# Optimization experiments

Hardware: AMD Instinct MI355X
Metric: run time of the kernel (lower is better)

Reference implementation:

```python
import jax, jax.numpy as jnp
import numpy as np

N = 20000   # nodes
E = 320000  # edges (before self-loops)
D = 256     # feature width (inChl = hdChl = outChl)
H = 4       # heads
C = D // H  # per-head channels = 64
NEG_SLOPE = 0.2
LN_EPS = 1e-5


def setup_inputs() -> dict:
    key = jax.random.key(0)
    ks = jax.random.split(key, 2 + 4 * 4)
    inp = {}
    inp["x"] = jax.random.normal(ks[0], (1, N, D), dtype=jnp.float32)
    inp["edge_index"] = jax.random.randint(ks[1], (2, E), 0, N, dtype=jnp.int32)
    s = 1.0 / np.sqrt(D)
    for i in range(4):
        k = 2 + 4 * i
        inp[f"Wl{i+1}"] = (jax.random.normal(ks[k], (D, H * C), dtype=jnp.float32) * s)
        inp[f"Wr{i+1}"] = (jax.random.normal(ks[k + 1], (D, H * C), dtype=jnp.float32) * s)
        inp[f"att{i+1}"] = (jax.random.normal(ks[k + 2], (H, C), dtype=jnp.float32) * s)
        inp[f"b{i+1}"] = jnp.zeros((H * C,), dtype=jnp.float32)
        inp[f"g{i+1}"] = jnp.ones((D,), dtype=jnp.float32)
        inp[f"be{i+1}"] = jnp.zeros((D,), dtype=jnp.float32)
    return inp


def _segment_softmax(scores, seg, num_segments):
    # scores: [E, H], per-destination softmax over incoming edges
    m = jax.ops.segment_max(scores, seg, num_segments=num_segments)
    e = jnp.exp(scores - m[seg])
    d = jax.ops.segment_sum(e, seg, num_segments=num_segments)
    return e / d[seg]


def _gatv2(x, src, dst, Wl, Wr, att, b):
    # GATv2Conv defaults: share_weights=False, concat=True, negative_slope=0.2
    n = x.shape[0]
    xl = (x @ Wl).reshape(n, H, C)  # source transform
    xr = (x @ Wr).reshape(n, H, C)  # target transform
    m = xl[src] + xr[dst]                                  # [E', H, C]
    e = jnp.sum(jax.nn.leaky_relu(m, NEG_SLOPE) * att, -1) # [E', H]
    alpha = _segment_softmax(e, dst, n)                    # [E', H]
    out = jax.ops.segment_sum(xl[src] * alpha[:, :, None], dst, num_segments=n)
    return out.reshape(n, H * C) + b


def _layernorm(x, g, b):
    mu = jnp.mean(x, -1, keepdims=True)
    var = jnp.mean(jnp.square(x - mu), -1, keepdims=True)
    return (x - mu) * jax.lax.rsqrt(var + LN_EPS) * g + b


def _forward(x, edge_index, layers):
    h = x[0]  # squeeze batch dim -> [N, D]
    n = h.shape[0]
    loop = jnp.arange(n, dtype=edge_index.dtype)
    src = jnp.concatenate([edge_index[0], loop])  # add_self_loops=True
    dst = jnp.concatenate([edge_index[1], loop])
    for (Wl, Wr, att, b, g, be) in layers:
        h = _gatv2(h, src, dst, Wl, Wr, att, b)
        h = jax.nn.relu(_layernorm(h, g, be))
    return h[None]  # unsqueeze -> [1, N, D]


def reference(x, edge_index,
              Wl1, Wr1, att1, b1, g1, be1,
              Wl2, Wr2, att2, b2, g2, be2,
              Wl3, Wr3, att3, b3, g3, be3,
              Wl4, Wr4, att4, b4, g4, be4):
    layers = [(Wl1, Wr1, att1, b1, g1, be1),
              (Wl2, Wr2, att2, b2, g2, be2),
              (Wl3, Wr3, att3, b3, g3, be3),
              (Wl4, Wr4, att4, b4, g4, be4)]
    return _forward(x, edge_index, layers)
```

## Files before the change

kernel.cpp:

```cpp
#include <hip/hip_runtime.h>
#include <math.h>

#define N_NODES 20000
#define E_EDGES 320000
#define EP (E_EDGES + N_NODES)
#define D 256
#define NHEAD 4
#define CH 64
#define NEG_SLOPE 0.2f
#define LN_EPS 1e-5f

typedef _Float16 half8_t __attribute__((ext_vector_type(8)));
typedef _Float16 half4_t __attribute__((ext_vector_type(4)));
typedef _Float16 half2_t __attribute__((ext_vector_type(2)));
typedef float   float4_t __attribute__((ext_vector_type(4)));
typedef int     iv4_t    __attribute__((ext_vector_type(4)));

#define SCATTER_BLOCKS ((EP + 255) / 256)
#define CONV_BLOCKS ((N_NODES * D / 4 + 255) / 256)

__device__ __forceinline__ void async_cp16(const void* g, void* l)
{
    __builtin_amdgcn_global_load_lds(
        (const __attribute__((address_space(1))) void*)g,
        (__attribute__((address_space(3))) void*)l, 16, 0, 0);
}

template<int CTRL>
__device__ __forceinline__ float dpp_add(float v) {
    int t = __builtin_amdgcn_update_dpp(0, __float_as_int(v), CTRL, 0xF, 0xF, true);
    return v + __int_as_float(t);
}
__device__ __forceinline__ float grp8_sum(float v) {
    v = dpp_add<0xB1>(v);
    v = dpp_add<0x4E>(v);
    v = dpp_add<0x141>(v);
    return v;
}

__device__ __forceinline__ iv4_t load_idx4(const int* p) {
    iv4_t v;
    __builtin_memcpy(&v, p, 16);
    return v;
}

__device__ __forceinline__ float dot_att8(half8_t t, const half2_t a0, const half2_t a1,
                                          const half2_t a2, const half2_t a3) {
    half2_t t01 = {t[0], t[1]}, t23 = {t[2], t[3]};
    half2_t t45 = {t[4], t[5]}, t67 = {t[6], t[7]};
    float v = __builtin_amdgcn_fdot2(t01, a0, 0.0f, false);
    v = __builtin_amdgcn_fdot2(t23, a1, v, false);
    v = __builtin_amdgcn_fdot2(t45, a2, v, false);
    return __builtin_amdgcn_fdot2(t67, a3, v, false);
}

struct WPtrs { const float* p[8]; };

__global__ __launch_bounds__(256)
void convert_hist_kernel(const float* __restrict__ x, _Float16* __restrict__ h16,
                         const int* __restrict__ ei, int* __restrict__ deg,
                         WPtrs wp, _Float16* __restrict__ Wt_all)
{
    if (blockIdx.x >= CONV_BLOCKS) {
        __shared__ float tile[64][65];
        int bz = blockIdx.x - CONV_BLOCKS;
        int bxi = bz & 3, byi = (bz >> 2) & 3, z = bz >> 4;
        const float* W = wp.p[z];
        _Float16* out = Wt_all + (size_t)z * 65536;
        int bx = bxi * 64, by = byi * 64;
        int t = threadIdx.x;
        #pragma unroll
        for (int i = 0; i < 16; ++i) {
            int idx = t + i * 256;
            int kk = idx >> 6, nn = idx & 63;
            tile[kk][nn] = W[(by + kk) * 256 + bx + nn];
        }
        __syncthreads();
        #pragma unroll
        for (int i = 0; i < 16; ++i) {
            int idx = t + i * 256;
            int nn = idx >> 6, kk = idx & 63;
            out[(bx + nn) * 256 + by + kk] = (_Float16)tile[kk][nn];
        }
        return;
    }
    int i = blockIdx.x * 256 + threadIdx.x;
    if (i < EP) {
        int dst = (i < E_EDGES) ? ei[E_EDGES + i] : (i - E_EDGES);
        atomicAdd(&deg[dst], 1);
    }
    if (i >= N_NODES * D / 4) return;
    float4 v = reinterpret_cast<const float4*>(x)[i];
    half4_t o;
    o.x = (_Float16)v.x; o.y = (_Float16)v.y; o.z = (_Float16)v.z; o.w = (_Float16)v.w;
    reinterpret_cast<half4_t*>(h16)[i] = o;
}

__global__ __launch_bounds__(1024)
void csr_scan_kernel(const int* __restrict__ deg, int* __restrict__ rowptr,
                     int* __restrict__ cursor, int* __restrict__ csr_src)
{
    __shared__ int buf[5120];
    __shared__ int wsum[16];
    __shared__ int carry_s;
    int t = threadIdx.x, lane = t & 63, w = t >> 6;
    if (t == 0) carry_s = 0;
    if (t < 8) csr_src[EP + t] = 0;

    for (int c = 0; c < 4; ++c) {
        int base = c * 5120;
        #pragma unroll
        for (int k = 0; k < 5; ++k) {
            int idx = base + k * 1024 + t;
            buf[k * 1024 + t] = (idx < N_NODES) ? deg[idx] : 0;
        }
        __syncthreads();
        int loc[5]; int s = 0;
        #pragma unroll
        for (int k = 0; k < 5; ++k) { loc[k] = buf[t * 5 + k]; s += loc[k]; }
        int x = s;
        #pragma unroll
        for (int o = 1; o < 64; o <<= 1) {
            int y = __shfl_up(x, o, 64);
            if (lane >= o) x += y;
        }
        if (lane == 63) wsum[w] = x;
        __syncthreads();
        if (t == 0) {
            int sa = carry_s;
            #pragma unroll
            for (int k = 0; k < 16; ++k) { int tmp = wsum[k]; wsum[k] = sa; sa += tmp; }
            carry_s = sa;
        }
        __syncthreads();
        int excl = wsum[w] + x - s;
        #pragma unroll
        for (int k = 0; k < 5; ++k) { buf[t * 5 + k] = excl; excl += loc[k]; }
        __syncthreads();
        #pragma unroll
        for (int k = 0; k < 5; ++k) {
            int idx = base + k * 1024 + t;
            if (idx < N_NODES) {
                int v = buf[k * 1024 + t];
                rowptr[idx] = v;
                cursor[idx] = v;
            }
        }
        __syncthreads();
    }
    if (t == 0) rowptr[N_NODES] = carry_s;
}

#define BM 128
#define BN 128
#define BK 64
#define EPAD2 72
__global__ __launch_bounds__(256)
void gemm_f16_kernel(const _Float16* __restrict__ A16, const _Float16* __restrict__ Wt,
                     _Float16* __restrict__ X0, _Float16* __restrict__ X1, int nrows,
                     const int* __restrict__ ei, int* __restrict__ cursor,
                     int* __restrict__ csr_src)
{
    const int b = blockIdx.x;
    if (b >= 640) {
        int e = (b - 640) * 256 + threadIdx.x;
        if (e >= EP) return;
        int src, dst;
        if (e < E_EDGES) { src = ei[e]; dst = ei[E_EDGES + e]; }
        else             { src = dst = e - E_EDGES; }
        int pos = atomicAdd(&cursor[dst], 1);
        csr_src[pos] = src;
        return;
    }

    const int pair = ((b >> 4) << 3) + (b & 7);
    const int z = (b >> 3) & 1;
    if (pair >= 314) return;
    const int yb = (pair >= 157) ? 1 : 0;
    const int xb = pair - yb * 157;

    const _Float16* W = Wt + z * 65536 + yb * (BN * 256);
    _Float16* X = z ? X1 : X0;
    const int row0 = xb * BM;
    const int col0 = yb * BN;

    __shared__ __align__(1024) char smem[BM * BK * 2 + BN * BK * 2];
    _Float16 (*As)[BK] = reinterpret_cast<_Float16 (*)[BK]>(smem);
    _Float16 (*Bs)[BK] = reinterpret_cast<_Float16 (*)[BK]>(smem + BM * BK * 2);
    _Float16* As_flat = reinterpret_cast<_Float16*>(smem);
    _Float16* Bs_flat = reinterpret_cast<_Float16*>(smem + BM * BK * 2);
    _Float16* ep = reinterpret_cast<_Float16*>(smem);

    const int tid  = threadIdx.x;
    const int wave = tid >> 6, lane = tid & 63;
    const int wy = wave >> 1, wx = wave & 1;
    const int quad = lane >> 4, l16 = lane & 15;

    float4_t acc[4][4];
    #pragma unroll
    for (int i = 0; i < 4; ++i)
        #pragma unroll
        for (int j = 0; j < 4; ++j) acc[i][j] = (float4_t)0.0f;

    const int r_in  = lane >> 3;
    const int c_in  = (lane & 7) * 8;

    #pragma unroll
    for (int k0 = 0; k0 < 256; k0 += BK) {
        #pragma unroll
        for (int j = 0; j < 4; ++j) {
            int ia  = wave * 4 + j;
            int row = ia * 8 + r_in;
            int gra = row0 + row;
            gra = (gra < nrows) ? gra : (nrows - 1);
            async_cp16(A16 + (size_t)gra * 256 + k0 + c_in, As_flat + ia * 512);
            async_cp16(W   + (size_t)row * 256 + k0 + c_in, Bs_flat + ia * 512);
        }
        __syncthreads();

        #pragma unroll
        for (int s = 0; s < 2; ++s) {
            half8_t af[4], bf[4];
            #pragma unroll
            for (int i = 0; i < 4; ++i)
                af[i] = *reinterpret_cast<const half8_t*>(&As[wy * 64 + i * 16 + l16][s * 32 + quad * 8]);
            #pragma unroll
            for (int j = 0; j < 4; ++j)
                bf[j] = *reinterpret_cast<const half8_t*>(&Bs[wx * 64 + j * 16 + l16][s * 32 + quad * 8]);
            #pragma unroll
            for (int i = 0; i < 4; ++i)
                #pragma unroll
                for (int j = 0; j < 4; ++j)
                    acc[i][j] = __builtin_amdgcn_mfma_f32_16x16x32_f16(af[i], bf[j], acc[i][j], 0, 0, 0);
        }
        __syncthreads();
    }

    _Float16* epw = ep + wave * 16 * EPAD2;
    #pragma unroll
    for (int it = 0; it < 4; ++it) {
        #pragma unroll
        for (int j = 0; j < 4; ++j)
            #pragma unroll
            for (int r = 0; r < 4; ++r)
                epw[(quad * 4 + r) * EPAD2 + j * 16 + l16] = (_Float16)acc[it][j][r];
        #pragma unroll
        for (int p = 0; p < 2; ++p) {
            int row = p * 8 + (lane >> 3);
            int col = (lane & 7) * 8;
            int gr = row0 + wy * 64 + it * 16 + row;
            half8_t v = *reinterpret_cast<const half8_t*>(&epw[row * EPAD2 + col]);
            if (gr < nrows)
                *reinterpret_cast<half8_t*>(X + gr * 256 + col0 + wx * 64 + col) = v;
        }
    }
}

__global__ __launch_bounds__(256)
void gat_fused_kernel(const _Float16* __restrict__ xl, const _Float16* __restrict__ xr,
                      const int* __restrict__ rowptr, const int* __restrict__ csr_src,
                      const float* __restrict__ att,
                      const float* __restrict__ bias, const float* __restrict__ g,
                      const float* __restrict__ be,
                      float* __restrict__ out32, _Float16* __restrict__ out16,
                      int write32)
{
    const int tid = threadIdx.x;
    const int w = tid >> 6, lane = tid & 63;
    const int n = blockIdx.x * 4 + w;
    const int hs  = lane >> 5;
    const int l32 = lane & 31;
    const int c0  = l32 * 8;
    const int start = rowptr[n], end = rowptr[n + 1];

    half8_t xrv = *reinterpret_cast<const half8_t*>(xr + (size_t)n * D + c0);
    half2_t at0, at1, at2, at3;
    {
        float4 a0 = *reinterpret_cast<const float4*>(att + c0);
        float4 a1 = *reinterpret_cast<const float4*>(att + c0 + 4);
        at0 = half2_t{(_Float16)a0.x, (_Float16)a0.y};
        at1 = half2_t{(_Float16)a0.z, (_Float16)a0.w};
        at2 = half2_t{(_Float16)a1.x, (_Float16)a1.y};
        at3 = half2_t{(_Float16)a1.z, (_Float16)a1.w};
    }
    const _Float16 slope = (_Float16)NEG_SLOPE;

    float den = 0.0f;
    float num[8];
    #pragma unroll
    for (int k = 0; k < 8; ++k) num[k] = 0.0f;

    int i = start;
    iv4_t nxt = load_idx4(csr_src + i + 4 * hs);
    for (; i + 8 <= end; i += 8) {
        iv4_t cur = nxt;
        half8_t h[4];
        #pragma unroll
        for (int j = 0; j < 4; ++j)
            h[j] = *reinterpret_cast<const half8_t*>(xl + (size_t)cur[j] * D + c0);
        nxt = load_idx4(csr_src + i + 8 + 4 * hs);
        float p[4];
        #pragma unroll
        for (int j = 0; j < 4; ++j) {
            half8_t t = h[j] + xrv;
            t = __builtin_elementwise_max(t, t * slope);
            p[j] = dot_att8(t, at0, at1, at2, at3);
        }
        #pragma unroll
        for (int j = 0; j < 4; ++j) p[j] = grp8_sum(p[j]);
        #pragma unroll
        for (int j = 0; j < 4; ++j) p[j] = __expf(p[j]);
        #pragma unroll
        for (int j = 0; j < 4; ++j) {
            den += p[j];
            #pragma unroll
            for (int k = 0; k < 8; ++k)
                num[k] = fmaf(p[j], (float)h[j][k], num[k]);
        }
    }
    if (i < end) {
        iv4_t cur = nxt;
        half8_t h[4];
        #pragma unroll
        for (int j = 0; j < 4; ++j)
            h[j] = *reinterpret_cast<const half8_t*>(xl + (size_t)cur[j] * D + c0);
        float p[4];
        #pragma unroll
        for (int j = 0; j < 4; ++j) {
            half8_t t = h[j] + xrv;
            t = __builtin_elementwise_max(t, t * slope);
            p[j] = dot_att8(t, at0, at1, at2, at3);
        }
        #pragma unroll
        for (int j = 0; j < 4; ++j) p[j] = grp8_sum(p[j]);
        #pragma unroll
        for (int j = 0; j < 4; ++j) {
            float pj = (i + 4 * hs + j < end) ? __expf(p[j]) : 0.0f;
            den += pj;
            #pragma unroll
            for (int k = 0; k < 8; ++k)
                num[k] = fmaf(pj, (float)h[j][k], num[k]);
        }
    }

    den += __shfl_xor(den, 32, 64);
    #pragma unroll
    for (int k = 0; k < 8; ++k) num[k] += __shfl_xor(num[k], 32, 64);

    float inv_den = 1.0f / den;
    float4 b0 = *reinterpret_cast<const float4*>(bias + c0);
    float4 b1 = *reinterpret_cast<const float4*>(bias + c0 + 4);
    float a[8];
    a[0] = fmaf(num[0], inv_den, b0.x);
    a[1] = fmaf(num[1], inv_den, b0.y);
    a[2] = fmaf(num[2], inv_den, b0.z);
    a[3] = fmaf(num[3], inv_den, b0.w);
    a[4] = fmaf(num[4], inv_den, b1.x);
    a[5] = fmaf(num[5], inv_den, b1.y);
    a[6] = fmaf(num[6], inv_den, b1.z);
    a[7] = fmaf(num[7], inv_den, b1.w);

    float wsum = 0.0f, wsq = 0.0f;
    #pragma unroll
    for (int k = 0; k < 8; ++k) { wsum += a[k]; wsq += a[k] * a[k]; }
    #pragma unroll
    for (int o = 1; o < 32; o <<= 1) {
        wsum += __shfl_xor(wsum, o, 64);
        wsq  += __shfl_xor(wsq,  o, 64);
    }
    float mu = wsum * (1.0f / 256.0f);
    float var = wsq * (1.0f / 256.0f) - mu * mu;
    float rstd = rsqrtf(var + LN_EPS);

    float4 g0 = *reinterpret_cast<const float4*>(g + c0);
    float4 g1 = *reinterpret_cast<const float4*>(g + c0 + 4);
    float4 e0 = *reinterpret_cast<const float4*>(be + c0);
    float4 e1 = *reinterpret_cast<const float4*>(be + c0 + 4);
    float o8[8];
    o8[0] = fmaxf((a[0] - mu) * rstd * g0.x + e0.x, 0.0f);
    o8[1] = fmaxf((a[1] - mu) * rstd * g0.y + e0.y, 0.0f);
    o8[2] = fmaxf((a[2] - mu) * rstd * g0.z + e0.z, 0.0f);
    o8[3] = fmaxf((a[3] - mu) * rstd * g0.w + e0.w, 0.0f);
    o8[4] = fmaxf((a[4] - mu) * rstd * g1.x + e1.x, 0.0f);
    o8[5] = fmaxf((a[5] - mu) * rstd * g1.y + e1.y, 0.0f);
    o8[6] = fmaxf((a[6] - mu) * rstd * g1.z + e1.z, 0.0f);
    o8[7] = fmaxf((a[7] - mu) * rstd * g1.w + e1.w, 0.0f);

    float s0 = hs ? o8[4] : o8[0];
    float s1 = hs ? o8[5] : o8[1];
    float s2 = hs ? o8[6] : o8[2];
    float s3 = hs ? o8[7] : o8[3];
    if (write32) {
        float4 ov = make_float4(s0, s1, s2, s3);
        *reinterpret_cast<float4*>(out32 + (size_t)n * D + c0 + 4 * hs) = ov;
    } else {
        half4_t ov;
        ov.x = (_Float16)s0; ov.y = (_Float16)s1; ov.z = (_Float16)s2; ov.w = (_Float16)s3;
        *reinterpret_cast<half4_t*>(out16 + (size_t)n * D + c0 + 4 * hs) = ov;
    }
}

extern "C" void kernel_launch(void* const* d_in, const int* in_sizes, int n_in,
                              void* d_out, int out_size, void* d_ws, size_t ws_size,
                              hipStream_t stream)
{
    const float* x  = (const float*)d_in[0];
    const int*   ei = (const int*)d_in[1];

    char* ws = (char*)d_ws;
    size_t off = 0;
    _Float16* h16   = (_Float16*)(ws + off); off += (size_t)N_NODES * D * 2;
    _Float16* xl    = (_Float16*)(ws + off); off += (size_t)N_NODES * D * 2;
    _Float16* xr    = (_Float16*)(ws + off); off += (size_t)N_NODES * D * 2;
    _Float16* WtA   = (_Float16*)(ws + off); off += (size_t)8 * 65536 * 2;
    int* rowptr     = (int*)(ws + off);      off += (size_t)(N_NODES + 32) * 4;
    int* cursor     = (int*)(ws + off);      off += (size_t)N_NODES * 4;
    int* csr_src    = (int*)(ws + off);      off += (size_t)(EP + 32) * 4;

    WPtrs wp;
    for (int l = 0; l < 4; ++l) {
        wp.p[2 * l + 0] = (const float*)d_in[2 + 6 * l + 0];
        wp.p[2 * l + 1] = (const float*)d_in[2 + 6 * l + 1];
    }

    hipMemsetAsync(cursor, 0, (size_t)N_NODES * 4, stream);
    convert_hist_kernel<<<CONV_BLOCKS + 128, 256, 0, stream>>>(x, h16, ei, cursor,
                                                               wp, WtA);
    csr_scan_kernel<<<1, 1024, 0, stream>>>(cursor, rowptr, cursor, csr_src);

    for (int l = 0; l < 4; ++l) {
        const float* att  = (const float*)d_in[2 + 6 * l + 2];
        const float* bias = (const float*)d_in[2 + 6 * l + 3];
        const float* g    = (const float*)d_in[2 + 6 * l + 4];
        const float* be   = (const float*)d_in[2 + 6 * l + 5];

        const int grid = (l == 0) ? (640 + SCATTER_BLOCKS) : 640;
        gemm_f16_kernel<<<grid, 256, 0, stream>>>(h16, WtA + (size_t)l * 131072,
                                                  xl, xr, N_NODES,
                                                  ei, cursor, csr_src);
        gat_fused_kernel<<<N_NODES / 4, 256, 0, stream>>>(xl, xr, rowptr, csr_src, att,
                                                          bias, g, be,
                                                          (float*)d_out, h16, (l == 3) ? 1 : 0);
    }
}
```

Measured before the change: 318.9 us.

## Fuse per-layer GEMM and GAT kernels into one persistent kernel with grid barriers

Replaces the eight per-layer launches (GEMM plus fused GAT for each of four layers) with a single persistent kernel of 768 blocks. Blocks loop over GEMM tiles and the layer-0 CSR scatter jobs, then over GAT node groups, separated by a software grid barrier built on atomics. This removes kernel launch gaps and tail effects between stages. In exchange it depends on all 768 blocks being co-resident (launch bounds ask for 3 blocks per CU) to avoid deadlock, and each barrier adds spin-wait cost. Work per block is also distributed with a stride loop instead of a hardware grid.

```diff
diff --git a/kernel.cpp b/kernel.cpp
--- a/kernel.cpp
+++ b/kernel.cpp
@@ -18,6 +18,7 @@
 
 #define SCATTER_BLOCKS ((EP + 255) / 256)
 #define CONV_BLOCKS ((N_NODES * D / 4 + 255) / 256)
+#define MEGA_GRID 768
 
 __device__ __forceinline__ void async_cp16(const void* g, void* l)
 {
@@ -54,13 +55,36 @@
     return __builtin_amdgcn_fdot2(t67, a3, v, false);
 }
 
+__device__ __forceinline__ void grid_barrier(int* bar)
+{
+    __syncthreads();
+    if (threadIdx.x == 0) {
+        __threadfence();
+        int gen = __hip_atomic_load(&bar[1], __ATOMIC_RELAXED, __HIP_MEMORY_SCOPE_AGENT);
+        int arrived = __hip_atomic_fetch_add(&bar[0], 1, __ATOMIC_ACQ_REL,
+                                             __HIP_MEMORY_SCOPE_AGENT) + 1;
+        if (arrived == MEGA_GRID) {
+            __hip_atomic_store(&bar[0], 0, __ATOMIC_RELAXED, __HIP_MEMORY_SCOPE_AGENT);
+            __hip_atomic_store(&bar[1], gen + 1, __ATOMIC_RELEASE, __HIP_MEMORY_SCOPE_AGENT);
+        } else {
+            while (__hip_atomic_load(&bar[1], __ATOMIC_RELAXED,
+                                     __HIP_MEMORY_SCOPE_AGENT) == gen)
+                __builtin_amdgcn_s_sleep(2);
+        }
+        __threadfence();
+    }
+    __syncthreads();
+}
+
 struct WPtrs { const float* p[8]; };
 
 __global__ __launch_bounds__(256)
 void convert_hist_kernel(const float* __restrict__ x, _Float16* __restrict__ h16,
                          const int* __restrict__ ei, int* __restrict__ deg,
-                         WPtrs wp, _Float16* __restrict__ Wt_all)
-{
+                         WPtrs wp, _Float16* __restrict__ Wt_all,
+                         int* __restrict__ bar)
+{
+    if (blockIdx.x == 0 && threadIdx.x < 4) bar[threadIdx.x] = 0;
     if (blockIdx.x >= CONV_BLOCKS) {
         __shared__ float tile[64][65];
         int bz = blockIdx.x - CONV_BLOCKS;
@@ -155,23 +179,12 @@
 #define BN 128
 #define BK 64
 #define EPAD2 72
-__global__ __launch_bounds__(256)
-void gemm_f16_kernel(const _Float16* __restrict__ A16, const _Float16* __restrict__ Wt,
-                     _Float16* __restrict__ X0, _Float16* __restrict__ X1, int nrows,
-                     const int* __restrict__ ei, int* __restrict__ cursor,
-                     int* __restrict__ csr_src)
-{
-    const int b = blockIdx.x;
-    if (b >= 640) {
-        int e = (b - 640) * 256 + threadIdx.x;
-        if (e >= EP) return;
-        int src, dst;
-        if (e < E_EDGES) { src = ei[e]; dst = ei[E_EDGES + e]; }
-        else             { src = dst = e - E_EDGES; }
-        int pos = atomicAdd(&cursor[dst], 1);
-        csr_src[pos] = src;
-        return;
-    }
+__device__ static void gemm_tile(int b, const _Float16* __restrict__ A16,
+                                 const _Float16* __restrict__ Wt,
+                                 _Float16* __restrict__ X0, _Float16* __restrict__ X1)
+{
+    __shared__ __align__(1024) char smem[BM * BK * 2 + BN * BK * 2];
+    __syncthreads();
 
     const int pair = ((b >> 4) << 3) + (b & 7);
     const int z = (b >> 3) & 1;
@@ -184,7 +197,6 @@
     const int row0 = xb * BM;
     const int col0 = yb * BN;
 
-    __shared__ __align__(1024) char smem[BM * BK * 2 + BN * BK * 2];
     _Float16 (*As)[BK] = reinterpret_cast<_Float16 (*)[BK]>(smem);
     _Float16 (*Bs)[BK] = reinterpret_cast<_Float16 (*)[BK]>(smem + BM * BK * 2);
     _Float16* As_flat = reinterpret_cast<_Float16*>(smem);
@@ -212,7 +224,7 @@
             int ia  = wave * 4 + j;
             int row = ia * 8 + r_in;
             int gra = row0 + row;
-            gra = (gra < nrows) ? gra : (nrows - 1);
+            gra = (gra < N_NODES) ? gra : (N_NODES - 1);
             async_cp16(A16 + (size_t)gra * 256 + k0 + c_in, As_flat + ia * 512);
             async_cp16(W   + (size_t)row * 256 + k0 + c_in, Bs_flat + ia * 512);
         }
@@ -250,24 +262,23 @@
             int col = (lane & 7) * 8;
             int gr = row0 + wy * 64 + it * 16 + row;
             half8_t v = *reinterpret_cast<const half8_t*>(&epw[row * EPAD2 + col]);
-            if (gr < nrows)
+            if (gr < N_NODES)
                 *reinterpret_cast<half8_t*>(X + gr * 256 + col0 + wx * 64 + col) = v;
         }
     }
 }
 
-__global__ __launch_bounds__(256)
-void gat_fused_kernel(const _Float16* __restrict__ xl, const _Float16* __restrict__ xr,
-                      const int* __restrict__ rowptr, const int* __restrict__ csr_src,
-                      const float* __restrict__ att,
-                      const float* __restrict__ bias, const float* __restrict__ g,
-                      const float* __restrict__ be,
-                      float* __restrict__ out32, _Float16* __restrict__ out16,
-                      int write32)
+__device__ static void gat4(int grp, const _Float16* __restrict__ xl,
+                            const _Float16* __restrict__ xr,
+                            const int* __restrict__ rowptr, const int* __restrict__ csr_src,
+                            const float* __restrict__ att, const float* __restrict__ bias,
+                            const float* __restrict__ g, const float* __restrict__ be,
+                            float* __restrict__ out32, _Float16* __restrict__ out16,
+                            int write32)
 {
     const int tid = threadIdx.x;
     const int w = tid >> 6, lane = tid & 63;
-    const int n = blockIdx.x * 4 + w;
+    const int n = grp * 4 + w;
     const int hs  = lane >> 5;
     const int l32 = lane & 31;
     const int c0  = l32 * 8;
@@ -400,6 +411,50 @@
     }
 }
 
+struct MegaParams {
+    const _Float16* h16c; _Float16* h16;
+    _Float16* xl; _Float16* xr;
+    const _Float16* WtA;
+    const int* rowptr; int* csr_src; int* cursor;
+    const int* ei;
+    const float* att[4]; const float* bias[4];
+    const float* g[4];   const float* be[4];
+    float* out32;
+    int* bar;
+};
+
+__global__ __launch_bounds__(256, 3)
+void mega_kernel(MegaParams p)
+{
+    #pragma unroll 1
+    for (int l = 0; l < 4; ++l) {
+        const _Float16* Wl = p.WtA + (size_t)l * 131072;
+        const int njobs = (l == 0) ? (640 + SCATTER_BLOCKS) : 640;
+        #pragma unroll 1
+        for (int j = blockIdx.x; j < njobs; j += MEGA_GRID) {
+            if (j < 640) {
+                gemm_tile(j, p.h16c, Wl, p.xl, p.xr);
+            } else {
+                int e = (j - 640) * 256 + threadIdx.x;
+                if (e < EP) {
+                    int src, dst;
+                    if (e < E_EDGES) { src = p.ei[e]; dst = p.ei[E_EDGES + e]; }
+                    else             { src = dst = e - E_EDGES; }
+                    int pos = atomicAdd(&p.cursor[dst], 1);
+                    p.csr_src[pos] = src;
+                }
+            }
+        }
+        grid_barrier(p.bar);
+        const int w32 = (l == 3) ? 1 : 0;
+        #pragma unroll 1
+        for (int grp = blockIdx.x; grp < N_NODES / 4; grp += MEGA_GRID)
+            gat4(grp, p.xl, p.xr, p.rowptr, p.csr_src,
+                 p.att[l], p.bias[l], p.g[l], p.be[l], p.out32, p.h16, w32);
+        if (l < 3) grid_barrier(p.bar);
+    }
+}
+
 extern "C" void kernel_launch(void* const* d_in, const int* in_sizes, int n_in,
                               void* d_out, int out_size, void* d_ws, size_t ws_size,
                               hipStream_t stream)
@@ -416,6 +471,7 @@
     int* rowptr     = (int*)(ws + off);      off += (size_t)(N_NODES + 32) * 4;
     int* cursor     = (int*)(ws + off);      off += (size_t)N_NODES * 4;
     int* csr_src    = (int*)(ws + off);      off += (size_t)(EP + 32) * 4;
+    int* bar        = (int*)(ws + off);      off += 64;
 
     WPtrs wp;
     for (int l = 0; l < 4; ++l) {
@@ -425,21 +481,20 @@
 
     hipMemsetAsync(cursor, 0, (size_t)N_NODES * 4, stream);
     convert_hist_kernel<<<CONV_BLOCKS + 128, 256, 0, stream>>>(x, h16, ei, cursor,
-                                                               wp, WtA);
+                                                               wp, WtA, bar);
     csr_scan_kernel<<<1, 1024, 0, stream>>>(cursor, rowptr, cursor, csr_src);
 
+    MegaParams mp;
+    mp.h16c = h16; mp.h16 = h16; mp.xl = xl; mp.xr = xr; mp.WtA = WtA;
+    mp.rowptr = rowptr; mp.csr_src = csr_src; mp.cursor = cursor; mp.ei = ei;
     for (int l = 0; l < 4; ++l) {
-        const float* att  = (const float*)d_in[2 + 6 * l + 2];
-        const float* bias = (const float*)d_in[2 + 6 * l + 3];
-        const float* g    = (const float*)d_in[2 + 6 * l + 4];
-        const float* be   = (const float*)d_in[2 + 6 * l + 5];
-
-        const int grid = (l == 0) ? (640 + SCATTER_BLOCKS) : 640;
-        gemm_f16_kernel<<<grid, 256, 0, stream>>>(h16, WtA + (size_t)l * 131072,
-                                                  xl, xr, N_NODES,
-                                                  ei, cursor, csr_src);
-        gat_fused_kernel<<<N_NODES / 4, 256, 0, stream>>>(xl, xr, rowptr, csr_src, att,
-                                                          bias, g, be,
-                                                          (float*)d_out, h16, (l == 3) ? 1 : 0);
-    }
-}
+        mp.att[l]  = (const float*)d_in[2 + 6 * l + 2];
+        mp.bias[l] = (const float*)d_in[2 + 6 * l + 3];
+        mp.g[l]    = (const float*)d_in[2 + 6 * l + 4];
+        mp.be[l]   = (const float*)d_in[2 + 6 * l + 5];
+    }
+    mp.out32 = (float*)d_out;
+    mp.bar = bar;
+
+    mega_kernel<<<MEGA_GRID, 256, 0, stream>>>(mp);
+}
```

Result: slower. 1.152 ms (+261.4%).
